# Optimization experiments

Hardware: AMD Instinct MI355X
Metric: run time of the kernel (lower is better)

## Reference

```python
import jax, jax.numpy as jnp
import numpy as np

N_USERS = 6144
N_ITEMS = 12288
N_NODES = N_USERS + N_ITEMS
D = 64
AVG_DEG = 32
NNZ = N_NODES * AVG_DEG
N_LAYERS = 2
K = 30  # module keeps top (k+1) per row


def setup_inputs() -> dict:
    key = jax.random.key(0)
    k1, k2, k3, k4, k5 = jax.random.split(key, 5)
    user_emb = 0.1 * jax.random.normal(k1, (N_USERS, D), dtype=jnp.float32)
    item_emb = 0.1 * jax.random.normal(k2, (N_ITEMS, D), dtype=jnp.float32)
    edge_row = jax.random.randint(k3, (NNZ,), 0, N_NODES, dtype=jnp.int32)
    edge_col = jax.random.randint(k4, (NNZ,), 0, N_NODES, dtype=jnp.int32)
    # normalized-adjacency-like values (positive, ~1/deg scale)
    edge_val = jax.random.uniform(k5, (NNZ,), dtype=jnp.float32) / AVG_DEG
    return {
        "user_emb": user_emb,
        "item_emb": item_emb,
        "edge_row": edge_row,
        "edge_col": edge_col,
        "edge_val": edge_val,
    }


def _spmm(edge_row, edge_col, edge_val, x):
    # y[r] = sum_{(r,c) in E} val * x[c]   -- torch.sparse.mm equivalent (COO)
    return jax.ops.segment_sum(edge_val[:, None] * x[edge_col], edge_row,
                               num_segments=N_NODES)


def reference(user_emb, item_emb, edge_row, edge_col, edge_val):
    # LightGCN propagation
    all_emb = jnp.concatenate([user_emb, item_emb], axis=0)  # [N, D]
    embs = [all_emb]
    for _ in range(N_LAYERS):
        all_emb = _spmm(edge_row, edge_col, edge_val, all_emb)
        embs.append(all_emb)
    light_out = jnp.mean(jnp.stack(embs, axis=1), axis=1)  # [N, D]

    items = light_out[N_USERS:]  # [N_ITEMS, D]
    # F.normalize(dim=1, p=2) with eps clamp
    norm = jnp.linalg.norm(items, axis=1, keepdims=True)
    items = items / jnp.maximum(norm, 1e-12)

    # dense pairwise similarity
    sim = items @ items.T  # [N_ITEMS, N_ITEMS]

    # top_k: keep top (k+1) values per row, zero elsewhere
    vals, idx = jax.lax.top_k(sim, K + 1)  # [N_ITEMS, K+1]
    rows = jnp.arange(sim.shape[0])[:, None]
    sparse_sim = jnp.zeros_like(sim).at[rows, idx].set(vals)

    # apply_non_linearity('relu', i) -> relu
    return jax.nn.relu(sparse_sim)
```

## Files before the change

kernel.cpp:

```cpp
#include <hip/hip_runtime.h>
#include <hip/hip_bf16.h>

#define N_USERS 6144
#define N_ITEMS 12288
#define N_NODES 18432
#define D 64
#define NNZ 589824
#define K_TOP 31
#define NCAND_MIN 96
#define CMAX 256
#define NB (N_NODES / 256)

using frag_ab = __attribute__((ext_vector_type(8))) short;
using frag_cd = __attribute__((ext_vector_type(4))) float;
using uint4_e = __attribute__((ext_vector_type(4))) unsigned;
using uint2_e = __attribute__((ext_vector_type(2))) unsigned;
using float4_e = __attribute__((ext_vector_type(4))) float;

__device__ inline unsigned f32_to_bf16_bits(float f) {
    unsigned b = __float_as_uint(f);
    return (b + 0x7FFFu + ((b >> 16) & 1u)) >> 16;
}
__device__ inline unsigned sim_to_u8(float v) {
    float e = rintf(fmaf(v, 127.5f, 127.5f));
    e = fminf(fmaxf(e, 0.f), 255.f);
    return (unsigned)(int)e;
}

__global__ void count_kernel(const int* __restrict__ er, int* __restrict__ cnt) {
    int e = blockIdx.x * 256 + threadIdx.x;
    atomicAdd(&cnt[er[e]], 1);
}

__global__ __launch_bounds__(256) void scanA_kernel(const int* __restrict__ cnt,
                                                    int* __restrict__ excl,
                                                    int* __restrict__ bsum) {
    __shared__ int sh[256];
    int t = threadIdx.x, b = blockIdx.x;
    int idx = b * 256 + t;
    int v = cnt[idx];
    sh[t] = v;
    __syncthreads();
    for (int off = 1; off < 256; off <<= 1) {
        int x = sh[t];
        int y = (t >= off) ? sh[t - off] : 0;
        __syncthreads();
        sh[t] = x + y;
        __syncthreads();
    }
    excl[idx] = sh[t] - v;
    if (t == 255) bsum[b] = sh[255];
}

__global__ __launch_bounds__(256) void scanC_kernel(const int* __restrict__ excl,
                                                    const int* __restrict__ bsum,
                                                    int* __restrict__ row_start,
                                                    int* __restrict__ cursor) {
    __shared__ int sb[NB];
    int t = threadIdx.x;
    if (t < NB) sb[t] = bsum[t];
    __syncthreads();
    if (t == 0) {
        int acc = 0;
        for (int i = 0; i < NB; ++i) { int v = sb[i]; sb[i] = acc; acc += v; }
    }
    __syncthreads();
    int idx = blockIdx.x * 256 + t;
    int v = excl[idx] + sb[idx >> 8];
    row_start[idx] = v;
    cursor[idx] = v;
    if (idx == 0) row_start[N_NODES] = NNZ;
}

__global__ void scatter_kernel(const int* __restrict__ er, const int* __restrict__ ec,
                               const float* __restrict__ ev,
                               int* __restrict__ cursor, int2* __restrict__ ep) {
    int e = blockIdx.x * 256 + threadIdx.x;
    int r = er[e];
    int pos = atomicAdd(&cursor[r], 1);
    ep[pos] = make_int2(ec[e], __float_as_int(ev[e]));
}

__global__ __launch_bounds__(256) void spmm_csr_kernel(const int* __restrict__ row_start,
                                                       const int2* __restrict__ ep,
                                                       const float* __restrict__ uemb,
                                                       const float* __restrict__ iemb,
                                                       double* __restrict__ y) {
    int t = threadIdx.x;
    int lane = t & 63, wave = t >> 6;
    int row = blockIdx.x * 4 + wave;
    int beg = row_start[row], end = row_start[row + 1];
    double a0 = 0.0, a1 = 0.0, a2 = 0.0, a3 = 0.0;
    int j = beg;
    int n4 = beg + ((end - beg) & ~3);
    const float* ishift = iemb - (size_t)N_USERS * D;
    for (; j < n4; j += 4) {
        int2 p0 = ep[j], p1 = ep[j + 1], p2 = ep[j + 2], p3 = ep[j + 3];
        const float* x0 = (p0.x < N_USERS) ? uemb : ishift;
        const float* x1 = (p1.x < N_USERS) ? uemb : ishift;
        const float* x2 = (p2.x < N_USERS) ? uemb : ishift;
        const float* x3 = (p3.x < N_USERS) ? uemb : ishift;
        a0 += (double)__int_as_float(p0.y) * (double)x0[(size_t)p0.x * D + lane];
        a1 += (double)__int_as_float(p1.y) * (double)x1[(size_t)p1.x * D + lane];
        a2 += (double)__int_as_float(p2.y) * (double)x2[(size_t)p2.x * D + lane];
        a3 += (double)__int_as_float(p3.y) * (double)x3[(size_t)p3.x * D + lane];
    }
    for (; j < end; ++j) {
        int2 p = ep[j];
        const float* x0 = (p.x < N_USERS) ? uemb : ishift;
        a0 += (double)__int_as_float(p.y) * (double)x0[(size_t)p.x * D + lane];
    }
    y[(size_t)row * D + lane] = (a0 + a1) + (a2 + a3);
}

__global__ __launch_bounds__(256) void spmm_norm_kernel(const int* __restrict__ row_start,
                                                        const int2* __restrict__ ep,
                                                        const float* __restrict__ iemb,
                                                        const double* __restrict__ e1,
                                                        double* __restrict__ xn64,
                                                        ushort* __restrict__ xh) {
    int t = threadIdx.x;
    int lane = t & 63, wave = t >> 6;
    int ir = blockIdx.x * 4 + wave;
    int row = ir + N_USERS;
    int beg = row_start[row], end = row_start[row + 1];
    double a0 = 0.0, a1 = 0.0, a2 = 0.0, a3 = 0.0;
    int j = beg;
    int n4 = beg + ((end - beg) & ~3);
    for (; j < n4; j += 4) {
        int2 p0 = ep[j], p1 = ep[j + 1], p2 = ep[j + 2], p3 = ep[j + 3];
        a0 += (double)__int_as_float(p0.y) * e1[(size_t)p0.x * D + lane];
        a1 += (double)__int_as_float(p1.y) * e1[(size_t)p1.x * D + lane];
        a2 += (double)__int_as_float(p2.y) * e1[(size_t)p2.x * D + lane];
        a3 += (double)__int_as_float(p3.y) * e1[(size_t)p3.x * D + lane];
    }
    for (; j < end; ++j) {
        int2 p = ep[j];
        a0 += (double)__int_as_float(p.y) * e1[(size_t)p.x * D + lane];
    }
    double e2v = (a0 + a1) + (a2 + a3);

    double e0v = (double)iemb[(size_t)ir * D + lane];
    double s = (e0v + e1[(size_t)row * D + lane] + e2v) / 3.0;
    double ss = s * s;
    #pragma unroll
    for (int off = 32; off; off >>= 1) ss += __shfl_xor(ss, off);
    double norm = sqrt(ss);
    double denom = fmax(norm, 1e-12);
    double v = s / denom;
    xn64[(size_t)ir * D + lane] = v;
    xh[(size_t)ir * D + lane] = (ushort)f32_to_bf16_bits((float)v);
}

#define LDS_STRIDE 72
#define OST_STRIDE 136
__global__ __launch_bounds__(256) void simgemm_kernel(const ushort* __restrict__ Xh,
                                                      unsigned char* __restrict__ Cu8) {
    __shared__ __align__(16) ushort S[2 * 128 * LDS_STRIDE];
    int bi = blockIdx.y, bj = blockIdx.x;
    if (bj < bi) return;
    ushort* Als = S;
    ushort* Bls = S + 128 * LDS_STRIDE;
    int t = threadIdx.x;

    #pragma unroll
    for (int p = 0; p < 4; ++p) {
        int u4 = t + 256 * p;
        int row = u4 >> 3;
        int seg = u4 & 7;
        *(uint4_e*)&Als[row * LDS_STRIDE + seg * 8] =
            *(const uint4_e*)&Xh[(size_t)(bi * 128 + row) * D + seg * 8];
        *(uint4_e*)&Bls[row * LDS_STRIDE + seg * 8] =
            *(const uint4_e*)&Xh[(size_t)(bj * 128 + row) * D + seg * 8];
    }
    __syncthreads();

    int lane = t & 63, wave = t >> 6;
    int wrow = (wave >> 1) * 64, wcol = (wave & 1) * 64;
    int ml = lane & 15, quad = lane >> 4;

    frag_cd acc[4][4] = {};
    #pragma unroll
    for (int s = 0; s < 2; ++s) {
        frag_ab af[4], bf[4];
        int koff = s * 32 + quad * 8;
        #pragma unroll
        for (int rt = 0; rt < 4; ++rt)
            af[rt] = *(const frag_ab*)&Als[(wrow + rt * 16 + ml) * LDS_STRIDE + koff];
        #pragma unroll
        for (int ct = 0; ct < 4; ++ct)
            bf[ct] = *(const frag_ab*)&Bls[(wcol + ct * 16 + ml) * LDS_STRIDE + koff];
        #pragma unroll
        for (int rt = 0; rt < 4; ++rt)
            #pragma unroll
            for (int ct = 0; ct < 4; ++ct)
                acc[rt][ct] = __builtin_amdgcn_mfma_f32_16x16x32_bf16(
                    af[rt], bf[ct], acc[rt][ct], 0, 0, 0);
    }
    __syncthreads();

    unsigned char* Ost  = (unsigned char*)S;
    unsigned char* Ost2 = (unsigned char*)S + 128 * OST_STRIDE;
    int offdiag = (bi != bj);
    #pragma unroll
    for (int rt = 0; rt < 4; ++rt) {
        #pragma unroll
        for (int ct = 0; ct < 4; ++ct) {
            int row = wrow + rt * 16 + quad * 4;
            int col = wcol + ct * 16 + ml;
            unsigned q0 = sim_to_u8(acc[rt][ct][0]);
            unsigned q1 = sim_to_u8(acc[rt][ct][1]);
            unsigned q2 = sim_to_u8(acc[rt][ct][2]);
            unsigned q3 = sim_to_u8(acc[rt][ct][3]);
            Ost[(row + 0) * OST_STRIDE + col] = (unsigned char)q0;
            Ost[(row + 1) * OST_STRIDE + col] = (unsigned char)q1;
            Ost[(row + 2) * OST_STRIDE + col] = (unsigned char)q2;
            Ost[(row + 3) * OST_STRIDE + col] = (unsigned char)q3;
            if (offdiag)
                *(unsigned*)&Ost2[col * OST_STRIDE + row] =
                    q0 | (q1 << 8) | (q2 << 16) | (q3 << 24);
        }
    }
    __syncthreads();

    const size_t base1 = (size_t)(bi * 128) * N_ITEMS + bj * 128;
    #pragma unroll
    for (int p = 0; p < 8; ++p) {
        int i = t + 256 * p;
        int row = i >> 4, seg = i & 15;
        uint2_e v = *(const uint2_e*)&Ost[row * OST_STRIDE + seg * 8];
        __builtin_nontemporal_store(v, (uint2_e*)(Cu8 + base1 + (size_t)row * N_ITEMS + seg * 8));
    }
    if (offdiag) {
        const size_t base2 = (size_t)(bj * 128) * N_ITEMS + bi * 128;
        #pragma unroll
        for (int p = 0; p < 8; ++p) {
            int i = t + 256 * p;
            int row = i >> 4, seg = i & 15;
            uint2_e v = *(const uint2_e*)&Ost2[row * OST_STRIDE + seg * 8];
            __builtin_nontemporal_store(v, (uint2_e*)(Cu8 + base2 + (size_t)row * N_ITEMS + seg * 8));
        }
    }
}

__global__ __launch_bounds__(256) void topk_kernel(const unsigned char* __restrict__ Cu8,
                                                   float* __restrict__ Cout,
                                                   const double* __restrict__ xn64) {
    __shared__ int s_red[4];
    __shared__ unsigned s_cnt;
    __shared__ int    candi[CMAX];
    __shared__ double candv[CMAX];
    __shared__ double s_xr[D];
    int t = threadIdx.x;
    int r = blockIdx.x;
    const uint4_e* Crow4 = (const uint4_e*)(Cu8 + (size_t)r * N_ITEMS);

    unsigned char u[48];
    #pragma unroll
    for (int j = 0; j < 3; ++j) {
        uint4_e f = __builtin_nontemporal_load(&Crow4[t + 256 * j]);
        #pragma unroll
        for (int q = 0; q < 4; ++q) {
            unsigned w = f[q];
            u[j * 16 + q * 4 + 0] = (unsigned char)(w & 0xFF);
            u[j * 16 + q * 4 + 1] = (unsigned char)((w >> 8) & 0xFF);
            u[j * 16 + q * 4 + 2] = (unsigned char)((w >> 16) & 0xFF);
            u[j * 16 + q * 4 + 3] = (unsigned char)(w >> 24);
        }
    }
    if (t < D) s_xr[t] = xn64[(size_t)r * D + t];

    int lo = 0, hi = 255;
    #pragma unroll
    for (int it = 0; it < 8; ++it) {
        int mid = (lo + hi + 1) >> 1;
        int c = 0;
        #pragma unroll
        for (int k = 0; k < 48; ++k) c += ((int)u[k] >= mid) ? 1 : 0;
        #pragma unroll
        for (int off = 32; off; off >>= 1) c += __shfl_down(c, off);
        if ((t & 63) == 0) s_red[t >> 6] = c;
        __syncthreads();
        int ctot = s_red[0] + s_red[1] + s_red[2] + s_red[3];
        __syncthreads();
        if (ctot >= NCAND_MIN) lo = mid; else hi = mid - 1;
    }
    int T = lo;

    if (t == 0) s_cnt = 0;
    __syncthreads();
    #pragma unroll
    for (int k = 0; k < 48; ++k) {
        if ((int)u[k] >= T) {
            unsigned pos = atomicAdd(&s_cnt, 1u);
            if (pos < CMAX) candi[pos] = 16 * (t + 256 * (k >> 4)) + (k & 15);
        }
    }
    __syncthreads();
    int c = (int)s_cnt; if (c > CMAX) c = CMAX;

    if (t < c) {
        const double* xc = xn64 + (size_t)candi[t] * D;
        double acc = 0.0;
        #pragma unroll 8
        for (int k = 0; k < D; ++k) acc += s_xr[k] * xc[k];
        candv[t] = acc;
    }
    __syncthreads();

    int   sel_idx = -1;
    float sel_val = 0.f;
    if (t < c) {
        double v = candv[t];
        int    id = candi[t];
        int rank = 0;
        for (int j = 0; j < c; ++j) {
            double vj = candv[j];
            rank += (vj > v || (vj == v && candi[j] < id)) ? 1 : 0;
        }
        if (rank < K_TOP) {
            sel_idx = id;
            sel_val = (v > 0.0) ? (float)v : 0.f;
        }
    }

    float4_e* Orow4 = (float4_e*)(Cout + (size_t)r * N_ITEMS);
    float4_e z = {0.f, 0.f, 0.f, 0.f};
    #pragma unroll
    for (int j = 0; j < 12; ++j)
        __builtin_nontemporal_store(z, &Orow4[t + 256 * j]);
    __syncthreads();
    if (sel_idx >= 0) Cout[(size_t)r * N_ITEMS + sel_idx] = sel_val;
}

extern "C" void kernel_launch(void* const* d_in, const int* in_sizes, int n_in,
                              void* d_out, int out_size, void* d_ws, size_t ws_size,
                              hipStream_t stream) {
    const float* user_emb = (const float*)d_in[0];
    const float* item_emb = (const float*)d_in[1];
    const int*   edge_row = (const int*)d_in[2];
    const int*   edge_col = (const int*)d_in[3];
    const float* edge_val = (const float*)d_in[4];
    float* C = (float*)d_out;

    double* e1d  = (double*)d_ws;
    double* xn64 = e1d + (size_t)N_NODES * D;
    int2*   ep   = (int2*)(xn64 + (size_t)N_ITEMS * D);
    ushort* xh   = (ushort*)(ep + NNZ);
    unsigned char* Cu8 = (unsigned char*)(xh + (size_t)N_ITEMS * D);
    int*  cnt       = (int*)(Cu8 + (size_t)N_ITEMS * N_ITEMS);
    int*  excl      = cnt + N_NODES;
    int*  row_start = excl + N_NODES;
    int*  cursor    = row_start + N_NODES + 1;
    int*  bsum      = cursor + N_NODES;

    (void)hipMemsetAsync(cnt, 0, N_NODES * sizeof(int), stream);

    count_kernel<<<NNZ / 256, 256, 0, stream>>>(edge_row, cnt);
    scanA_kernel<<<N_NODES / 256, 256, 0, stream>>>(cnt, excl, bsum);
    scanC_kernel<<<N_NODES / 256, 256, 0, stream>>>(excl, bsum, row_start, cursor);
    scatter_kernel<<<NNZ / 256, 256, 0, stream>>>(edge_row, edge_col, edge_val, cursor, ep);

    spmm_csr_kernel<<<N_NODES / 4, 256, 0, stream>>>(row_start, ep, user_emb, item_emb, e1d);
    spmm_norm_kernel<<<N_ITEMS / 4, 256, 0, stream>>>(row_start, ep, item_emb, e1d, xn64, xh);

    dim3 ggrid(N_ITEMS / 128, N_ITEMS / 128);
    simgemm_kernel<<<ggrid, 256, 0, stream>>>(xh, Cu8);

    topk_kernel<<<N_ITEMS, 256, 0, stream>>>(Cu8, C, xn64);
}
```

Baseline: 890.8 us.

## Replace materialized u8 similarity matrix with two-pass GEMM and per-row candidate emission

Drops the full 12288x12288 uint8 similarity matrix. A first GEMM pass records only per-64-column-tile row maxima, a small kernel turns those into a per-row threshold, and a second GEMM pass recomputes the tiles and atomically appends entries above that threshold to a per-row candidate buffer. The finalize kernel re-selects from the candidates with fp64 rescoring and falls back to a full recompute when a row overflows the buffer. This removes about 150 MB of global writes and reads in exchange for computing the GEMM twice and paying for global atomics.

```diff
diff --git a/kernel.cpp b/kernel.cpp
--- a/kernel.cpp
+++ b/kernel.cpp
@@ -7,14 +7,14 @@
 #define D 64
 #define NNZ 589824
 #define K_TOP 31
-#define NCAND_MIN 96
-#define CMAX 256
+#define TSEL 96
+#define CAP_CAND 1024
+#define NTILES 192
 #define NB (N_NODES / 256)
 
 using frag_ab = __attribute__((ext_vector_type(8))) short;
 using frag_cd = __attribute__((ext_vector_type(4))) float;
 using uint4_e = __attribute__((ext_vector_type(4))) unsigned;
-using uint2_e = __attribute__((ext_vector_type(2))) unsigned;
 using float4_e = __attribute__((ext_vector_type(4))) float;
 
 __device__ inline unsigned f32_to_bf16_bits(float f) {
@@ -153,9 +153,9 @@
 }
 
 #define LDS_STRIDE 72
-#define OST_STRIDE 136
-__global__ __launch_bounds__(256) void simgemm_kernel(const ushort* __restrict__ Xh,
-                                                      unsigned char* __restrict__ Cu8) {
+
+__global__ __launch_bounds__(256) void gemm_rowmax_kernel(const ushort* __restrict__ Xh,
+                                                          unsigned char* __restrict__ rowmax) {
     __shared__ __align__(16) ushort S[2 * 128 * LDS_STRIDE];
     int bi = blockIdx.y, bj = blockIdx.x;
     if (bj < bi) return;
@@ -197,130 +197,276 @@
                 acc[rt][ct] = __builtin_amdgcn_mfma_f32_16x16x32_bf16(
                     af[rt], bf[ct], acc[rt][ct], 0, 0, 0);
     }
+
+    unsigned m1[4][4];
+    #pragma unroll
+    for (int rt = 0; rt < 4; ++rt)
+        #pragma unroll
+        for (int r = 0; r < 4; ++r) {
+            unsigned q = sim_to_u8(acc[rt][0][r]);
+            #pragma unroll
+            for (int ct = 1; ct < 4; ++ct) {
+                unsigned q2 = sim_to_u8(acc[rt][ct][r]);
+                if (q2 > q) q = q2;
+            }
+            m1[rt][r] = q;
+        }
+    #pragma unroll
+    for (int mask = 1; mask <= 8; mask <<= 1)
+        #pragma unroll
+        for (int rt = 0; rt < 4; ++rt)
+            #pragma unroll
+            for (int r = 0; r < 4; ++r) {
+                unsigned o = (unsigned)__shfl_xor((int)m1[rt][r], mask);
+                if (o > m1[rt][r]) m1[rt][r] = o;
+            }
+    if (ml == 0) {
+        int tidx = bj * 2 + (wcol >> 6);
+        #pragma unroll
+        for (int rt = 0; rt < 4; ++rt)
+            #pragma unroll
+            for (int r = 0; r < 4; ++r)
+                rowmax[(size_t)(bi * 128 + wrow + rt * 16 + quad * 4 + r) * NTILES + tidx] =
+                    (unsigned char)m1[rt][r];
+    }
+
+    if (bi != bj) {
+        unsigned m2[4];
+        #pragma unroll
+        for (int ct = 0; ct < 4; ++ct) {
+            unsigned q = 0;
+            #pragma unroll
+            for (int rt = 0; rt < 4; ++rt)
+                #pragma unroll
+                for (int r = 0; r < 4; ++r) {
+                    unsigned q2 = sim_to_u8(acc[rt][ct][r]);
+                    if (q2 > q) q = q2;
+                }
+            m2[ct] = q;
+        }
+        #pragma unroll
+        for (int mask = 16; mask <= 32; mask <<= 1)
+            #pragma unroll
+            for (int ct = 0; ct < 4; ++ct) {
+                unsigned o = (unsigned)__shfl_xor((int)m2[ct], mask);
+                if (o > m2[ct]) m2[ct] = o;
+            }
+        if (quad == 0) {
+            int tidx = bi * 2 + (wrow >> 6);
+            #pragma unroll
+            for (int ct = 0; ct < 4; ++ct)
+                rowmax[(size_t)(bj * 128 + wcol + ct * 16 + ml) * NTILES + tidx] =
+                    (unsigned char)m2[ct];
+        }
+    }
+}
+
+__global__ __launch_bounds__(256) void rowthresh_kernel(const unsigned char* __restrict__ rowmax,
+                                                        unsigned char* __restrict__ Trow) {
+    int t = threadIdx.x;
+    int lane = t & 63;
+    int row = blockIdx.x * 4 + (t >> 6);
+    const unsigned char* rm = rowmax + (size_t)row * NTILES;
+    int a = rm[lane], b = rm[lane + 64], c = rm[lane + 128];
+    int lo = 0, hi = 255;
+    #pragma unroll
+    for (int it = 0; it < 8; ++it) {
+        int mid = (lo + hi + 1) >> 1;
+        int cc = (a >= mid) + (b >= mid) + (c >= mid);
+        #pragma unroll
+        for (int off = 32; off; off >>= 1) cc += __shfl_xor(cc, off);
+        if (cc >= TSEL) lo = mid; else hi = mid - 1;
+    }
+    if (lane == 0) Trow[row] = (unsigned char)lo;
+}
+
+__global__ __launch_bounds__(256) void gemm_emit_kernel(const ushort* __restrict__ Xh,
+                                                        const unsigned char* __restrict__ Trow,
+                                                        int* __restrict__ ccnt,
+                                                        unsigned* __restrict__ candbuf) {
+    __shared__ __align__(16) ushort S[2 * 128 * LDS_STRIDE];
+    __shared__ unsigned char sTrow[128], sTcol[128];
+    int bi = blockIdx.y, bj = blockIdx.x;
+    if (bj < bi) return;
+    ushort* Als = S;
+    ushort* Bls = S + 128 * LDS_STRIDE;
+    int t = threadIdx.x;
+
+    if (t < 128) {
+        sTrow[t] = Trow[bi * 128 + t];
+        sTcol[t] = Trow[bj * 128 + t];
+    }
+    #pragma unroll
+    for (int p = 0; p < 4; ++p) {
+        int u4 = t + 256 * p;
+        int row = u4 >> 3;
+        int seg = u4 & 7;
+        *(uint4_e*)&Als[row * LDS_STRIDE + seg * 8] =
+            *(const uint4_e*)&Xh[(size_t)(bi * 128 + row) * D + seg * 8];
+        *(uint4_e*)&Bls[row * LDS_STRIDE + seg * 8] =
+            *(const uint4_e*)&Xh[(size_t)(bj * 128 + row) * D + seg * 8];
+    }
     __syncthreads();
 
-    unsigned char* Ost  = (unsigned char*)S;
-    unsigned char* Ost2 = (unsigned char*)S + 128 * OST_STRIDE;
+    int lane = t & 63, wave = t >> 6;
+    int wrow = (wave >> 1) * 64, wcol = (wave & 1) * 64;
+    int ml = lane & 15, quad = lane >> 4;
+
+    frag_cd acc[4][4] = {};
+    #pragma unroll
+    for (int s = 0; s < 2; ++s) {
+        frag_ab af[4], bf[4];
+        int koff = s * 32 + quad * 8;
+        #pragma unroll
+        for (int rt = 0; rt < 4; ++rt)
+            af[rt] = *(const frag_ab*)&Als[(wrow + rt * 16 + ml) * LDS_STRIDE + koff];
+        #pragma unroll
+        for (int ct = 0; ct < 4; ++ct)
+            bf[ct] = *(const frag_ab*)&Bls[(wcol + ct * 16 + ml) * LDS_STRIDE + koff];
+        #pragma unroll
+        for (int rt = 0; rt < 4; ++rt)
+            #pragma unroll
+            for (int ct = 0; ct < 4; ++ct)
+                acc[rt][ct] = __builtin_amdgcn_mfma_f32_16x16x32_bf16(
+                    af[rt], bf[ct], acc[rt][ct], 0, 0, 0);
+    }
+
     int offdiag = (bi != bj);
     #pragma unroll
     for (int rt = 0; rt < 4; ++rt) {
         #pragma unroll
         for (int ct = 0; ct < 4; ++ct) {
-            int row = wrow + rt * 16 + quad * 4;
-            int col = wcol + ct * 16 + ml;
-            unsigned q0 = sim_to_u8(acc[rt][ct][0]);
-            unsigned q1 = sim_to_u8(acc[rt][ct][1]);
-            unsigned q2 = sim_to_u8(acc[rt][ct][2]);
-            unsigned q3 = sim_to_u8(acc[rt][ct][3]);
-            Ost[(row + 0) * OST_STRIDE + col] = (unsigned char)q0;
-            Ost[(row + 1) * OST_STRIDE + col] = (unsigned char)q1;
-            Ost[(row + 2) * OST_STRIDE + col] = (unsigned char)q2;
-            Ost[(row + 3) * OST_STRIDE + col] = (unsigned char)q3;
-            if (offdiag)
-                *(unsigned*)&Ost2[col * OST_STRIDE + row] =
-                    q0 | (q1 << 8) | (q2 << 16) | (q3 << 24);
-        }
-    }
-    __syncthreads();
-
-    const size_t base1 = (size_t)(bi * 128) * N_ITEMS + bj * 128;
-    #pragma unroll
-    for (int p = 0; p < 8; ++p) {
-        int i = t + 256 * p;
-        int row = i >> 4, seg = i & 15;
-        uint2_e v = *(const uint2_e*)&Ost[row * OST_STRIDE + seg * 8];
-        __builtin_nontemporal_store(v, (uint2_e*)(Cu8 + base1 + (size_t)row * N_ITEMS + seg * 8));
-    }
-    if (offdiag) {
-        const size_t base2 = (size_t)(bj * 128) * N_ITEMS + bi * 128;
-        #pragma unroll
-        for (int p = 0; p < 8; ++p) {
-            int i = t + 256 * p;
-            int row = i >> 4, seg = i & 15;
-            uint2_e v = *(const uint2_e*)&Ost2[row * OST_STRIDE + seg * 8];
-            __builtin_nontemporal_store(v, (uint2_e*)(Cu8 + base2 + (size_t)row * N_ITEMS + seg * 8));
-        }
-    }
-}
-
-__global__ __launch_bounds__(256) void topk_kernel(const unsigned char* __restrict__ Cu8,
-                                                   float* __restrict__ Cout,
-                                                   const double* __restrict__ xn64) {
+            #pragma unroll
+            for (int r = 0; r < 4; ++r) {
+                unsigned q = sim_to_u8(acc[rt][ct][r]);
+                int row1 = wrow + rt * 16 + quad * 4 + r;
+                int col1 = wcol + ct * 16 + ml;
+                if (q >= (unsigned)sTrow[row1]) {
+                    int g = bi * 128 + row1;
+                    int pos = atomicAdd(&ccnt[g], 1);
+                    if (pos < CAP_CAND)
+                        candbuf[(size_t)g * CAP_CAND + pos] = (q << 16) | (unsigned)(bj * 128 + col1);
+                }
+                if (offdiag && q >= (unsigned)sTcol[col1]) {
+                    int g = bj * 128 + col1;
+                    int pos = atomicAdd(&ccnt[g], 1);
+                    if (pos < CAP_CAND)
+                        candbuf[(size_t)g * CAP_CAND + pos] = (q << 16) | (unsigned)(bi * 128 + row1);
+                }
+            }
+        }
+    }
+}
+
+__global__ __launch_bounds__(256) void finalize_kernel(const int* __restrict__ ccnt,
+                                                       const unsigned* __restrict__ candbuf,
+                                                       const double* __restrict__ xn64,
+                                                       float* __restrict__ Cout) {
+    __shared__ int      candi[CAP_CAND];
+    __shared__ double   candv[CAP_CAND];
+    __shared__ double   s_xr[D];
     __shared__ int s_red[4];
     __shared__ unsigned s_cnt;
-    __shared__ int    candi[CMAX];
-    __shared__ double candv[CMAX];
-    __shared__ double s_xr[D];
     int t = threadIdx.x;
     int r = blockIdx.x;
-    const uint4_e* Crow4 = (const uint4_e*)(Cu8 + (size_t)r * N_ITEMS);
-
-    unsigned char u[48];
-    #pragma unroll
-    for (int j = 0; j < 3; ++j) {
-        uint4_e f = __builtin_nontemporal_load(&Crow4[t + 256 * j]);
-        #pragma unroll
-        for (int q = 0; q < 4; ++q) {
-            unsigned w = f[q];
-            u[j * 16 + q * 4 + 0] = (unsigned char)(w & 0xFF);
-            u[j * 16 + q * 4 + 1] = (unsigned char)((w >> 8) & 0xFF);
-            u[j * 16 + q * 4 + 2] = (unsigned char)((w >> 16) & 0xFF);
-            u[j * 16 + q * 4 + 3] = (unsigned char)(w >> 24);
-        }
-    }
     if (t < D) s_xr[t] = xn64[(size_t)r * D + t];
-
-    int lo = 0, hi = 255;
-    #pragma unroll
-    for (int it = 0; it < 8; ++it) {
-        int mid = (lo + hi + 1) >> 1;
-        int c = 0;
-        #pragma unroll
-        for (int k = 0; k < 48; ++k) c += ((int)u[k] >= mid) ? 1 : 0;
-        #pragma unroll
-        for (int off = 32; off; off >>= 1) c += __shfl_down(c, off);
-        if ((t & 63) == 0) s_red[t >> 6] = c;
-        __syncthreads();
-        int ctot = s_red[0] + s_red[1] + s_red[2] + s_red[3];
-        __syncthreads();
-        if (ctot >= NCAND_MIN) lo = mid; else hi = mid - 1;
-    }
-    int T = lo;
-
-    if (t == 0) s_cnt = 0;
-    __syncthreads();
-    #pragma unroll
-    for (int k = 0; k < 48; ++k) {
-        if ((int)u[k] >= T) {
-            unsigned pos = atomicAdd(&s_cnt, 1u);
-            if (pos < CMAX) candi[pos] = 16 * (t + 256 * (k >> 4)) + (k & 15);
-        }
-    }
-    __syncthreads();
-    int c = (int)s_cnt; if (c > CMAX) c = CMAX;
-
-    if (t < c) {
-        const double* xc = xn64 + (size_t)candi[t] * D;
-        double acc = 0.0;
-        #pragma unroll 8
-        for (int k = 0; k < D; ++k) acc += s_xr[k] * xc[k];
-        candv[t] = acc;
-    }
-    __syncthreads();
-
-    int   sel_idx = -1;
-    float sel_val = 0.f;
-    if (t < c) {
-        double v = candv[t];
-        int    id = candi[t];
+    int cval = ccnt[r];
+    int c;
+
+    if (cval <= CAP_CAND) {
+        for (int i = t; i < cval; i += 256) candi[i] = (int)candbuf[(size_t)r * CAP_CAND + i];
+        c = cval;
+        __syncthreads();
+        int lo = 0, hi = 255;
+        for (int it = 0; it < 8; ++it) {
+            int mid = (lo + hi + 1) >> 1;
+            int cc = 0;
+            for (int i = t; i < c; i += 256) cc += ((candi[i] >> 16) >= mid);
+            #pragma unroll
+            for (int off = 32; off; off >>= 1) cc += __shfl_down(cc, off);
+            if ((t & 63) == 0) s_red[t >> 6] = cc;
+            __syncthreads();
+            int ctot = s_red[0] + s_red[1] + s_red[2] + s_red[3];
+            __syncthreads();
+            if (ctot >= TSEL) lo = mid; else hi = mid - 1;
+        }
+        int Tp = lo;
+        for (int i = t; i < c; i += 256) {
+            if ((candi[i] >> 16) >= Tp) {
+                const double* xc = xn64 + (size_t)(candi[i] & 0xFFFF) * D;
+                double a = 0.0;
+                #pragma unroll 8
+                for (int k = 0; k < D; ++k) a += s_xr[k] * xc[k];
+                candv[i] = a;
+            } else {
+                candv[i] = -1.0e300;
+            }
+        }
+        __syncthreads();
+    } else {
+        __syncthreads();
+        unsigned char u[48];
+        #pragma unroll
+        for (int j = 0; j < 48; ++j) {
+            int col = t + 256 * j;
+            const double* xc = xn64 + (size_t)col * D;
+            double a = 0.0;
+            #pragma unroll 8
+            for (int k = 0; k < D; ++k) a += s_xr[k] * xc[k];
+            u[j] = (unsigned char)sim_to_u8((float)a);
+        }
+        int lo = 0, hi = 255;
+        for (int it = 0; it < 8; ++it) {
+            int mid = (lo + hi + 1) >> 1;
+            int cc = 0;
+            #pragma unroll
+            for (int j = 0; j < 48; ++j) cc += ((int)u[j] >= mid);
+            #pragma unroll
+            for (int off = 32; off; off >>= 1) cc += __shfl_down(cc, off);
+            if ((t & 63) == 0) s_red[t >> 6] = cc;
+            __syncthreads();
+            int ctot = s_red[0] + s_red[1] + s_red[2] + s_red[3];
+            __syncthreads();
+            if (ctot >= TSEL) lo = mid; else hi = mid - 1;
+        }
+        int T2 = lo;
+        if (t == 0) s_cnt = 0;
+        __syncthreads();
+        #pragma unroll
+        for (int j = 0; j < 48; ++j) {
+            if ((int)u[j] >= T2) {
+                int col = t + 256 * j;
+                const double* xc = xn64 + (size_t)col * D;
+                double a = 0.0;
+                #pragma unroll 8
+                for (int k = 0; k < D; ++k) a += s_xr[k] * xc[k];
+                unsigned pos = atomicAdd(&s_cnt, 1u);
+                if (pos < CAP_CAND) {
+                    candi[pos] = ((int)u[j] << 16) | col;
+                    candv[pos] = a;
+                }
+            }
+        }
+        __syncthreads();
+        c = (int)s_cnt; if (c > CAP_CAND) c = CAP_CAND;
+    }
+
+    int   sel_col[4];
+    float sel_val[4];
+    int nsel = 0;
+    for (int i = t; i < c; i += 256) {
+        double v = candv[i];
+        int col_i = candi[i] & 0xFFFF;
         int rank = 0;
         for (int j = 0; j < c; ++j) {
             double vj = candv[j];
-            rank += (vj > v || (vj == v && candi[j] < id)) ? 1 : 0;
+            int cj = candi[j] & 0xFFFF;
+            rank += (vj > v || (vj == v && cj < col_i)) ? 1 : 0;
         }
         if (rank < K_TOP) {
-            sel_idx = id;
-            sel_val = (v > 0.0) ? (float)v : 0.f;
+            sel_col[nsel] = col_i;
+            sel_val[nsel] = (v > 0.0) ? (float)v : 0.f;
+            ++nsel;
         }
     }
 
@@ -330,7 +476,8 @@
     for (int j = 0; j < 12; ++j)
         __builtin_nontemporal_store(z, &Orow4[t + 256 * j]);
     __syncthreads();
-    if (sel_idx >= 0) Cout[(size_t)r * N_ITEMS + sel_idx] = sel_val;
+    for (int s = 0; s < nsel; ++s)
+        Cout[(size_t)r * N_ITEMS + sel_col[s]] = sel_val[s];
 }
 
 extern "C" void kernel_launch(void* const* d_in, const int* in_sizes, int n_in,
@@ -346,15 +493,18 @@
     double* e1d  = (double*)d_ws;
     double* xn64 = e1d + (size_t)N_NODES * D;
     int2*   ep   = (int2*)(xn64 + (size_t)N_ITEMS * D);
-    ushort* xh   = (ushort*)(ep + NNZ);
-    unsigned char* Cu8 = (unsigned char*)(xh + (size_t)N_ITEMS * D);
-    int*  cnt       = (int*)(Cu8 + (size_t)N_ITEMS * N_ITEMS);
-    int*  excl      = cnt + N_NODES;
+    unsigned* candbuf = (unsigned*)(ep + NNZ);
+    int*  cnt       = (int*)(candbuf + (size_t)N_ITEMS * CAP_CAND);
+    int*  ccnt      = cnt + N_NODES;
+    int*  excl      = ccnt + N_ITEMS;
     int*  row_start = excl + N_NODES;
     int*  cursor    = row_start + N_NODES + 1;
     int*  bsum      = cursor + N_NODES;
-
-    (void)hipMemsetAsync(cnt, 0, N_NODES * sizeof(int), stream);
+    ushort* xh      = (ushort*)(bsum + 128);
+    unsigned char* rowmax = (unsigned char*)(xh + (size_t)N_ITEMS * D);
+    unsigned char* Trow   = rowmax + (size_t)N_ITEMS * NTILES;
+
+    (void)hipMemsetAsync(cnt, 0, (N_NODES + N_ITEMS) * sizeof(int), stream);
 
     count_kernel<<<NNZ / 256, 256, 0, stream>>>(edge_row, cnt);
     scanA_kernel<<<N_NODES / 256, 256, 0, stream>>>(cnt, excl, bsum);
@@ -365,7 +515,9 @@
     spmm_norm_kernel<<<N_ITEMS / 4, 256, 0, stream>>>(row_start, ep, item_emb, e1d, xn64, xh);
 
     dim3 ggrid(N_ITEMS / 128, N_ITEMS / 128);
-    simgemm_kernel<<<ggrid, 256, 0, stream>>>(xh, Cu8);
-
-    topk_kernel<<<N_ITEMS, 256, 0, stream>>>(Cu8, C, xn64);
-}
+    gemm_rowmax_kernel<<<ggrid, 256, 0, stream>>>(xh, rowmax);
+    rowthresh_kernel<<<N_ITEMS / 4, 256, 0, stream>>>(rowmax, Trow);
+    gemm_emit_kernel<<<ggrid, 256, 0, stream>>>(xh, Trow, ccnt, candbuf);
+
+    finalize_kernel<<<N_ITEMS, 256, 0, stream>>>(ccnt, candbuf, xn64, C);
+}
```

Result: slower. 1.410 ms (+58.3%).
